# Performance work log

Measured on AMD Instinct MI355X. Metric: run time of the kernel, lower is better.

Reference implementation:

```python
import jax, jax.numpy as jnp
import numpy as np

B, S, D, H, K, F = 4, 2048, 512, 8, 512, 2048
EPS = 1e-3  # keras LayerNormalization default epsilon


def setup_inputs() -> dict:
    key = jax.random.key(0)
    ks = jax.random.split(key, 12)
    s = 0.02
    return {
        "x":  jax.random.normal(ks[0], (B, S, D), jnp.float32),
        "Wq": jax.random.normal(ks[1], (D, H, K), jnp.float32) * s,
        "bq": jnp.zeros((H, K), jnp.float32),
        "Wk": jax.random.normal(ks[2], (D, H, K), jnp.float32) * s,
        "bk": jnp.zeros((H, K), jnp.float32),
        "Wv": jax.random.normal(ks[3], (D, H, K), jnp.float32) * s,
        "bv": jnp.zeros((H, K), jnp.float32),
        "Wo": jax.random.normal(ks[4], (H, K, D), jnp.float32) * s,
        "bo": jnp.zeros((D,), jnp.float32),
        "W1": jax.random.normal(ks[5], (D, F), jnp.float32) * s,
        "b1": jnp.zeros((F,), jnp.float32),
        "W2": jax.random.normal(ks[6], (F, D), jnp.float32) * s,
        "b2": jnp.zeros((D,), jnp.float32),
        "g1": jnp.ones((D,), jnp.float32),
        "be1": jnp.zeros((D,), jnp.float32),
        "g2": jnp.ones((D,), jnp.float32),
        "be2": jnp.zeros((D,), jnp.float32),
    }


def _layernorm(x, g, b):
    m = jnp.mean(x, axis=-1, keepdims=True)
    v = jnp.mean(jnp.square(x - m), axis=-1, keepdims=True)
    return (x - m) * jax.lax.rsqrt(v + EPS) * g + b


def reference(x, Wq, bq, Wk, bk, Wv, bv, Wo, bo, W1, b1, W2, b2, g1, be1, g2, be2):
    # --- multi-head attention with tridiagonal band mask (window=1) ---
    q = jnp.einsum("bsd,dhk->bshk", x, Wq) + bq
    k = jnp.einsum("bsd,dhk->bshk", x, Wk) + bk
    v = jnp.einsum("bsd,dhk->bshk", x, Wv) + bv
    scores = jnp.einsum("bqhk,bshk->bhqs", q, k) / jnp.sqrt(jnp.float32(K))
    idx = jnp.arange(S)
    band = jnp.abs(idx[:, None] - idx[None, :]) <= 1  # band_part(ones,1,1)
    scores = jnp.where(band[None, None], scores, jnp.float32(-1e9))
    probs = jax.nn.softmax(scores, axis=-1)
    ctx = jnp.einsum("bhqs,bshk->bqhk", probs, v)
    attn = jnp.einsum("bqhk,hkd->bqd", ctx, Wo) + bo
    # dropout is identity at inference
    out1 = _layernorm(x + attn, g1, be1)
    # --- FFN: Dense(gelu) -> Dense ---
    h = jax.nn.gelu(out1 @ W1 + b1, approximate=False)
    ffn = h @ W2 + b2
    return _layernorm(out1 + ffn, g2, be2)
```

## Files before the change

### kernel.cpp

```cpp
#include <hip/hip_runtime.h>
#include <hip/hip_bf16.h>
#include <math.h>

#define B_ 4
#define S_ 2048
#define D_ 512
#define H_ 8
#define K_ 512
#define F_ 2048
#define NT 8192
#define HK 4096

typedef __attribute__((ext_vector_type(8))) short bf16x8;
typedef __attribute__((ext_vector_type(4))) float f32x4;
typedef unsigned short u16;

__device__ __forceinline__ float bits2f(u16 b) {
  union { unsigned u; float f; } c; c.u = ((unsigned)b) << 16; return c.f;
}
__device__ __forceinline__ u16 f2bfbits(float f) {
  union { float f; unsigned u; } c; c.f = f;
  unsigned r = c.u + 0x7fffu + ((c.u >> 16) & 1u);
  return (u16)(r >> 16);
}

__device__ __forceinline__ void gload16(const void* g, void* lds) {
  __builtin_amdgcn_global_load_lds(
      (const __attribute__((address_space(1))) unsigned int*)g,
      (__attribute__((address_space(3))) unsigned int*)lds, 16, 0, 0);
}

__global__ __launch_bounds__(256) void prep_all(
    const float* __restrict__ Wq, const float* __restrict__ Wk,
    const float* __restrict__ Wv, const float* __restrict__ Wo,
    const float* __restrict__ W1, const float* __restrict__ W2,
    const float* __restrict__ bv, const float* __restrict__ x,
    u16* __restrict__ wq_nt, u16* __restrict__ wk_nt,
    u16* __restrict__ mtwv, u16* __restrict__ wot,
    u16* __restrict__ w1t, u16* __restrict__ w2t,
    float* __restrict__ biascat, u16* __restrict__ xb) {
  const int id = blockIdx.x;
  const int tid = threadIdx.x;
  __shared__ float tile[32][33];
  if (id < 6144) {
    const int tx = tid & 31;
    const int ty = tid >> 5;
    const float* src; u16* dst;
    int rb, cb, ldin, ldout;
    if (id < 2048) {
      int rem = id; rb = (rem & 15) * 32; cb = (rem >> 4) * 32;
      src = Wv; ldin = HK; dst = mtwv + (size_t)4096 * 512; ldout = D_;
    } else if (id < 4096) {
      int rem = id - 2048; rb = (rem >> 4) * 32; cb = (rem & 15) * 32;
      src = Wo; ldin = D_; dst = wot; ldout = HK;
    } else if (id < 5120) {
      int rem = id - 4096; rb = (rem & 15) * 32; cb = (rem >> 4) * 32;
      src = W1; ldin = F_; dst = w1t; ldout = D_;
    } else {
      int rem = id - 5120; rb = (rem >> 4) * 32; cb = (rem & 15) * 32;
      src = W2; ldin = D_; dst = w2t; ldout = F_;
    }
    for (int i = ty; i < 32; i += 8)
      tile[i][tx] = src[(size_t)(rb + i) * ldin + cb + tx];
    __syncthreads();
    for (int i = ty; i < 32; i += 8)
      dst[(size_t)(cb + i) * ldout + rb + tx] = f2bfbits(tile[tx][i]);
  } else if (id < 14336) {
    const float* s; u16* d; int base;
    if (id < 8192)       { s = Wq; d = wq_nt; base = id - 6144; }
    else if (id < 10240) { s = Wk; d = wk_nt; base = id - 8192; }
    else                 { s = x;  d = xb;    base = id - 10240; }
    int i = base * 256 + tid;
    float4 f = ((const float4*)s)[i];
    ushort4 o;
    o.x = f2bfbits(f.x); o.y = f2bfbits(f.y);
    o.z = f2bfbits(f.z); o.w = f2bfbits(f.w);
    ((ushort4*)d)[i] = o;
  } else {
    int i = (id - 14336) * 256 + tid;
    float4 o = make_float4(0.f, 0.f, 0.f, 0.f);
    if (i >= 1024) o = ((const float4*)bv)[i - 1024];
    ((float4*)biascat)[i] = o;
  }
}

template <int BIAS, int GELU, int OUTBF, int BATCH>
__global__ __launch_bounds__(256) void gemm128d(const u16* __restrict__ A, int lda,
                                                size_t aZ,
                                                const u16* __restrict__ Bt, int ldb,
                                                size_t bZ,
                                                const float* __restrict__ bias,
                                                float* __restrict__ Cf, size_t zstride,
                                                u16* __restrict__ Cb, int ldc,
                                                size_t cZ, int kslice) {
  __shared__ short lds[2][16384];
  const int tid = threadIdx.x;
  const int lane = tid & 63;
  const int wave = tid >> 6;
  const int bm = blockIdx.x * 128;
  const int bn = blockIdx.y * 128;
  const int z = blockIdx.z;
  const int k0 = BATCH ? 0 : z * kslice;
  if (BATCH) { A += z * aZ; Bt += z * bZ; }

  const int wr = (wave >> 1) * 64;
  const int wc = (wave & 1) * 64;

  f32x4 acc[4][4] = {};

  const int srow = wave * 8 + (lane >> 3);
  const int scol = ((lane & 7) ^ (lane >> 3)) * 8;
  const u16* ag = A + (size_t)(bm + srow) * lda + scol;
  const u16* bg = Bt + (size_t)(bn + srow) * ldb + scol;
  const int ldsbase = wave * 8 * 64;

  auto STAGE = [&](int buf, int kt) {
    short* sA = &lds[buf][0];
    short* sB = &lds[buf][8192];
#pragma unroll
    for (int r = 0; r < 4; ++r)
      gload16(ag + (size_t)(r * 32) * lda + kt, sA + ldsbase + r * 32 * 64);
#pragma unroll
    for (int r = 0; r < 4; ++r)
      gload16(bg + (size_t)(r * 32) * ldb + kt, sB + ldsbase + r * 32 * 64);
  };

  auto COMPUTE = [&](int buf) {
    const short* sA = &lds[buf][0];
    const short* sB = &lds[buf][8192];
#pragma unroll
    for (int ks = 0; ks < 2; ++ks) {
      const int kos = (ks * 32 + (lane >> 4) * 8) ^ ((lane & 7) << 3);
      bf16x8 a[4], b[4];
#pragma unroll
      for (int m = 0; m < 4; ++m)
        a[m] = *(const bf16x8*)&sA[(wr + m * 16 + (lane & 15)) * 64 + kos];
#pragma unroll
      for (int n = 0; n < 4; ++n)
        b[n] = *(const bf16x8*)&sB[(wc + n * 16 + (lane & 15)) * 64 + kos];
#pragma unroll
      for (int m = 0; m < 4; ++m)
#pragma unroll
        for (int n = 0; n < 4; ++n)
          acc[m][n] = __builtin_amdgcn_mfma_f32_16x16x32_bf16(a[m], b[n], acc[m][n], 0, 0, 0);
    }
  };

  const int nt = kslice >> 6;
  STAGE(0, k0);
  __syncthreads();
  int cur = 0;
  for (int t = 0; t + 1 < nt; ++t) {
    STAGE(cur ^ 1, k0 + (t + 1) * 64);
    COMPUTE(cur);
    __syncthreads();
    cur ^= 1;
  }
  COMPUTE(cur);

  float* Cfz = Cf + (BATCH ? 0 : (size_t)z * zstride);
  u16* Cbz = Cb + (BATCH ? (size_t)z * cZ : 0);
#pragma unroll
  for (int m = 0; m < 4; ++m) {
    const int row0 = bm + wr + m * 16 + (lane >> 4) * 4;
#pragma unroll
    for (int n = 0; n < 4; ++n) {
      const int col = bn + wc + n * 16 + (lane & 15);
      float badd = BIAS ? bias[col] : 0.f;
      f32x4 a4 = acc[m][n];
#pragma unroll
      for (int r = 0; r < 4; ++r) {
        float vv = a4[r] + badd;
        if (GELU) vv = 0.5f * vv * (1.f + erff(vv * 0.70710678118f));
        const int row = row0 + r;
        if (OUTBF) Cbz[(size_t)row * ldc + col] = f2bfbits(vv);
        else Cfz[(size_t)row * ldc + col] = vv;
      }
    }
  }
}

__global__ __launch_bounds__(256) void attn2(u16* yv, const u16* __restrict__ xb) {
  const int t = blockIdx.x;
  const int s = t & (S_ - 1);
  const int tid = threadIdx.x;
  const int lane = tid & 63;
  const int wave = tid >> 6;
  __shared__ float sSc[8][3];
  __shared__ float sP[8][3];
  const u16* yrow = yv + (size_t)t * 8192;

#pragma unroll
  for (int i = 0; i < 6; ++i) {
    const int didx = wave * 6 + i;
    const int h = didx / 3, j = didx % 3;
    const bool valid = !((j == 0 && s == 0) || (j == 2 && s == S_ - 1));
    float d = 0.f;
    if (valid) {
      const int tj = t + j - 1;
      bf16x8 y8 = *(const bf16x8*)&yrow[h * 512 + lane * 8];
      bf16x8 x8 = *(const bf16x8*)&xb[(size_t)tj * D_ + lane * 8];
#pragma unroll
      for (int e = 0; e < 8; ++e) d += bits2f((u16)y8[e]) * bits2f((u16)x8[e]);
    }
    for (int m = 32; m >= 1; m >>= 1) d += __shfl_xor(d, m);
    if (lane == 0) sSc[h][j] = valid ? d : -1e30f;
  }
  __syncthreads();
  if (tid < 8) {
    const float scale = 0.044194173824159f;
    float s0 = sSc[tid][0], s1 = sSc[tid][1], s2 = sSc[tid][2];
    s0 = (s0 > -1e29f) ? s0 * scale : -1e30f;
    s1 = s1 * scale;
    s2 = (s2 > -1e29f) ? s2 * scale : -1e30f;
    float mx = fmaxf(s0, fmaxf(s1, s2));
    float p0 = (s0 > -1e29f) ? expf(s0 - mx) : 0.f;
    float p1 = expf(s1 - mx);
    float p2 = (s2 > -1e29f) ? expf(s2 - mx) : 0.f;
    float inv = 1.f / (p0 + p1 + p2);
    sP[tid][0] = p0 * inv; sP[tid][1] = p1 * inv; sP[tid][2] = p2 * inv;
  }
  __syncthreads();
  const int c0 = tid * 16;
  const int h = tid >> 5;
  const float p0 = sP[h][0], p1 = sP[h][1], p2 = sP[h][2];
  const int tm = t - (s > 0 ? 1 : 0);
  const int tp = t + (s < S_ - 1 ? 1 : 0);
  const u16* v0r = yv + (size_t)tm * 8192 + 4096;
  const u16* v1r = yv + (size_t)t * 8192 + 4096;
  const u16* v2r = yv + (size_t)tp * 8192 + 4096;
#pragma unroll
  for (int c = 0; c < 2; ++c) {
    const int col = c0 + c * 8;
    bf16x8 a = *(const bf16x8*)&v0r[col];
    bf16x8 b = *(const bf16x8*)&v1r[col];
    bf16x8 cc = *(const bf16x8*)&v2r[col];
    bf16x8 o;
#pragma unroll
    for (int e = 0; e < 8; ++e)
      o[e] = (short)f2bfbits(p0 * bits2f((u16)a[e]) + p1 * bits2f((u16)b[e]) +
                             p2 * bits2f((u16)cc[e]));
    *(bf16x8*)&yv[(size_t)t * 8192 + col] = o;
  }
}

__global__ __launch_bounds__(256) void resid_ln(const float* __restrict__ xres,
                                                const float* __restrict__ parts,
                                                int nparts, size_t pstride,
                                                size_t prowstride,
                                                const float* __restrict__ bias,
                                                const float* __restrict__ gamma,
                                                const float* __restrict__ beta,
                                                float* __restrict__ outf,
                                                u16* __restrict__ outb) {
  const int row = blockIdx.x;
  const int tid = threadIdx.x;
  const size_t base = (size_t)row * D_;
  float2 xv = ((const float2*)(xres + base))[tid];
  float y0 = xv.x, y1 = xv.y;
  for (int p = 0; p < nparts; ++p) {
    const float* pr = parts + p * pstride + (size_t)row * prowstride;
    float2 pv = ((const float2*)pr)[tid];
    y0 += pv.x; y1 += pv.y;
  }
  if (bias) {
    float2 bv = ((const float2*)bias)[tid];
    y0 += bv.x; y1 += bv.y;
  }
  float s = y0 + y1, ss = y0 * y0 + y1 * y1;
  for (int m = 32; m >= 1; m >>= 1) { s += __shfl_xor(s, m); ss += __shfl_xor(ss, m); }
  __shared__ float red[8];
  const int wave = tid >> 6, lane = tid & 63;
  if (lane == 0) { red[wave] = s; red[4 + wave] = ss; }
  __syncthreads();
  s = red[0] + red[1] + red[2] + red[3];
  ss = red[4] + red[5] + red[6] + red[7];
  const float mean = s * (1.f / D_);
  const float var = ss * (1.f / D_) - mean * mean;
  const float rstd = rsqrtf(var + 1e-3f);
  float2 gv = ((const float2*)gamma)[tid];
  float2 bev = ((const float2*)beta)[tid];
  float o0 = (y0 - mean) * rstd * gv.x + bev.x;
  float o1 = (y1 - mean) * rstd * gv.y + bev.y;
  if (outf) { float2 of; of.x = o0; of.y = o1; ((float2*)(outf + base))[tid] = of; }
  if (outb) { ushort2 ob; ob.x = f2bfbits(o0); ob.y = f2bfbits(o1); ((ushort2*)(outb + base))[tid] = ob; }
}

extern "C" void kernel_launch(void* const* d_in, const int* in_sizes, int n_in,
                              void* d_out, int out_size, void* d_ws, size_t ws_size,
                              hipStream_t stream) {
  const float* x  = (const float*)d_in[0];
  const float* Wq = (const float*)d_in[1];
  const float* Wk = (const float*)d_in[3];
  const float* Wv = (const float*)d_in[5];
  const float* bv = (const float*)d_in[6];
  const float* Wo = (const float*)d_in[7];
  const float* bo = (const float*)d_in[8];
  const float* W1 = (const float*)d_in[9];
  const float* b1 = (const float*)d_in[10];
  const float* W2 = (const float*)d_in[11];
  const float* b2 = (const float*)d_in[12];
  const float* g1 = (const float*)d_in[13];
  const float* be1 = (const float*)d_in[14];
  const float* g2 = (const float*)d_in[15];
  const float* be2 = (const float*)d_in[16];
  float* out = (float*)d_out;

  char* w = (char*)d_ws;
  size_t o = 0;
  auto nxt = [&](size_t bytes) -> char* {
    char* p = w + o;
    o += (bytes + 255) & ~(size_t)255;
    return p;
  };
  u16* xb     = (u16*)nxt((size_t)NT * D_ * 2);
  u16* wq_nt  = (u16*)nxt((size_t)D_ * HK * 2);
  u16* wk_nt  = (u16*)nxt((size_t)D_ * HK * 2);
  u16* wot    = (u16*)nxt((size_t)D_ * HK * 2);
  u16* w1t    = (u16*)nxt((size_t)F_ * D_ * 2);
  u16* w2t    = (u16*)nxt((size_t)D_ * F_ * 2);
  u16* mtwv   = (u16*)nxt((size_t)8192 * 512 * 2);
  float* biascat = (float*)nxt((size_t)8192 * 4);
  u16* yv     = (u16*)nxt((size_t)NT * 8192 * 2);
  float* out1f = (float*)nxt((size_t)NT * D_ * 4);
  u16* out1b   = (u16*)nxt((size_t)NT * D_ * 2);
  float* woPart = (float*)(yv + 4096);
  u16* hb = (u16*)((char*)yv + 33554432);
  float* ffnP = (float*)((char*)yv + 100663296);

  prep_all<<<dim3(14344), 256, 0, stream>>>(Wq, Wk, Wv, Wo, W1, W2, bv, x,
                                            wq_nt, wk_nt, mtwv, wot, w1t, w2t,
                                            biascat, xb);

  gemm128d<0, 0, 1, 1><<<dim3(4, 4, 8), 256, 0, stream>>>(
      wk_nt, HK, 512, wq_nt, HK, 512, nullptr,
      nullptr, 0, mtwv, 512, (size_t)512 * 512, 512);

  gemm128d<1, 0, 1, 0><<<dim3(64, 64, 1), 256, 0, stream>>>(
      xb, D_, 0, mtwv, 512, 0, biascat, nullptr, 0, yv, 8192, 0, 512);

  attn2<<<dim3(NT), 256, 0, stream>>>(yv, xb);

  gemm128d<0, 0, 0, 0><<<dim3(64, 4, 2), 256, 0, stream>>>(
      yv, 8192, 0, wot, HK, 0, nullptr, woPart, 512, nullptr, 4096, 0, 2048);

  resid_ln<<<dim3(NT), 256, 0, stream>>>(x, woPart, 2, 512, 4096, bo,
                                         g1, be1, out1f, out1b);

  gemm128d<1, 1, 1, 0><<<dim3(64, 16, 1), 256, 0, stream>>>(
      out1b, D_, 0, w1t, D_, 0, b1, nullptr, 0, hb, F_, 0, 512);

  gemm128d<0, 0, 0, 0><<<dim3(64, 4, 2), 256, 0, stream>>>(
      hb, F_, 0, w2t, F_, 0, nullptr, ffnP, (size_t)NT * D_, nullptr, D_, 0, 1024);

  resid_ln<<<dim3(NT), 256, 0, stream>>>(out1f, ffnP, 2, (size_t)NT * D_, D_, b2,
                                         g2, be2, out, nullptr);

  (void)in_sizes; (void)n_in; (void)out_size; (void)ws_size;
}
```

Measured before the change: 303.1 us.

## Fold Wo into value projection and drop separate output-projection GEMM

Precomputes Wv·Wo per head as a combined weight inside the batched weight GEMM, so the large projection GEMM emits per-head value vectors already projected to model dimension. Attention then mixes the three band neighbours across all heads into a single 512-wide fp32 row, which removes the separate Wo GEMM over the 4096-wide context. The bv·Wo bias is folded in by a small new kernel. The big projection GEMM stays the same size, and the extra precomputed products add a little bf16 rounding.

```diff
diff --git a/kernel.cpp b/kernel.cpp
--- a/kernel.cpp
+++ b/kernel.cpp
@@ -34,30 +34,27 @@
     const float* __restrict__ Wq, const float* __restrict__ Wk,
     const float* __restrict__ Wv, const float* __restrict__ Wo,
     const float* __restrict__ W1, const float* __restrict__ W2,
-    const float* __restrict__ bv, const float* __restrict__ x,
+    const float* __restrict__ x,
     u16* __restrict__ wq_nt, u16* __restrict__ wk_nt,
-    u16* __restrict__ mtwv, u16* __restrict__ wot,
+    u16* __restrict__ wv_nt, u16* __restrict__ wot,
     u16* __restrict__ w1t, u16* __restrict__ w2t,
-    float* __restrict__ biascat, u16* __restrict__ xb) {
+    u16* __restrict__ xb) {
   const int id = blockIdx.x;
   const int tid = threadIdx.x;
   __shared__ float tile[32][33];
-  if (id < 6144) {
+  if (id < 4096) {
     const int tx = tid & 31;
     const int ty = tid >> 5;
     const float* src; u16* dst;
     int rb, cb, ldin, ldout;
     if (id < 2048) {
-      int rem = id; rb = (rem & 15) * 32; cb = (rem >> 4) * 32;
-      src = Wv; ldin = HK; dst = mtwv + (size_t)4096 * 512; ldout = D_;
-    } else if (id < 4096) {
-      int rem = id - 2048; rb = (rem >> 4) * 32; cb = (rem & 15) * 32;
+      int rem = id; rb = (rem >> 4) * 32; cb = (rem & 15) * 32;
       src = Wo; ldin = D_; dst = wot; ldout = HK;
-    } else if (id < 5120) {
-      int rem = id - 4096; rb = (rem & 15) * 32; cb = (rem >> 4) * 32;
+    } else if (id < 3072) {
+      int rem = id - 2048; rb = (rem & 15) * 32; cb = (rem >> 4) * 32;
       src = W1; ldin = F_; dst = w1t; ldout = D_;
     } else {
-      int rem = id - 5120; rb = (rem >> 4) * 32; cb = (rem & 15) * 32;
+      int rem = id - 3072; rb = (rem >> 4) * 32; cb = (rem & 15) * 32;
       src = W2; ldin = D_; dst = w2t; ldout = F_;
     }
     for (int i = ty; i < 32; i += 8)
@@ -65,10 +62,11 @@
     __syncthreads();
     for (int i = ty; i < 32; i += 8)
       dst[(size_t)(cb + i) * ldout + rb + tx] = f2bfbits(tile[tx][i]);
-  } else if (id < 14336) {
+  } else {
     const float* s; u16* d; int base;
-    if (id < 8192)       { s = Wq; d = wq_nt; base = id - 6144; }
-    else if (id < 10240) { s = Wk; d = wk_nt; base = id - 8192; }
+    if (id < 6144)       { s = Wq; d = wq_nt; base = id - 4096; }
+    else if (id < 8192)  { s = Wk; d = wk_nt; base = id - 6144; }
+    else if (id < 10240) { s = Wv; d = wv_nt; base = id - 8192; }
     else                 { s = x;  d = xb;    base = id - 10240; }
     int i = base * 256 + tid;
     float4 f = ((const float4*)s)[i];
@@ -76,11 +74,25 @@
     o.x = f2bfbits(f.x); o.y = f2bfbits(f.y);
     o.z = f2bfbits(f.z); o.w = f2bfbits(f.w);
     ((ushort4*)d)[i] = o;
-  } else {
-    int i = (id - 14336) * 256 + tid;
-    float4 o = make_float4(0.f, 0.f, 0.f, 0.f);
-    if (i >= 1024) o = ((const float4*)bv)[i - 1024];
-    ((float4*)biascat)[i] = o;
+  }
+}
+
+__global__ __launch_bounds__(256) void cbias(const float* __restrict__ bv,
+                                             const float* __restrict__ Wo,
+                                             float* __restrict__ biascat) {
+  const int lane = threadIdx.x & 63;
+  const int out = blockIdx.x * 4 + (threadIdx.x >> 6);
+  const int h = out >> 9, dp = out & 511;
+  float a = 0.f;
+#pragma unroll
+  for (int i = 0; i < 8; ++i) {
+    const int k = lane * 8 + i;
+    a += bv[h * 512 + k] * Wo[(size_t)(h * 512 + k) * D_ + dp];
+  }
+  for (int m = 32; m >= 1; m >>= 1) a += __shfl_xor(a, m);
+  if (lane == 0) {
+    biascat[4096 + out] = a;
+    biascat[out] = 0.f;
   }
 }
 
@@ -89,6 +101,9 @@
                                                 size_t aZ,
                                                 const u16* __restrict__ Bt, int ldb,
                                                 size_t bZ,
+                                                const u16* __restrict__ A2,
+                                                const u16* __restrict__ Bt2,
+                                                int zsplit,
                                                 const float* __restrict__ bias,
                                                 float* __restrict__ Cf, size_t zstride,
                                                 u16* __restrict__ Cb, int ldc,
@@ -101,7 +116,10 @@
   const int bn = blockIdx.y * 128;
   const int z = blockIdx.z;
   const int k0 = BATCH ? 0 : z * kslice;
-  if (BATCH) { A += z * aZ; Bt += z * bZ; }
+  if (BATCH) {
+    if (z < zsplit) { A += (size_t)z * aZ; Bt += (size_t)z * bZ; }
+    else { A = A2 + (size_t)(z - zsplit) * aZ; Bt = Bt2 + (size_t)(z - zsplit) * bZ; }
+  }
 
   const int wr = (wave >> 1) * 64;
   const int wc = (wave & 1) * 64;
@@ -180,7 +198,7 @@
   }
 }
 
-__global__ __launch_bounds__(256) void attn2(u16* yv, const u16* __restrict__ xb) {
+__global__ __launch_bounds__(256) void attn3(u16* yz, const u16* __restrict__ xb) {
   const int t = blockIdx.x;
   const int s = t & (S_ - 1);
   const int tid = threadIdx.x;
@@ -188,7 +206,7 @@
   const int wave = tid >> 6;
   __shared__ float sSc[8][3];
   __shared__ float sP[8][3];
-  const u16* yrow = yv + (size_t)t * 8192;
+  const u16* yrow = yz + (size_t)t * 8192;
 
 #pragma unroll
   for (int i = 0; i < 6; ++i) {
@@ -221,27 +239,24 @@
     sP[tid][0] = p0 * inv; sP[tid][1] = p1 * inv; sP[tid][2] = p2 * inv;
   }
   __syncthreads();
-  const int c0 = tid * 16;
-  const int h = tid >> 5;
-  const float p0 = sP[h][0], p1 = sP[h][1], p2 = sP[h][2];
+  const int d0 = tid * 2;
   const int tm = t - (s > 0 ? 1 : 0);
   const int tp = t + (s < S_ - 1 ? 1 : 0);
-  const u16* v0r = yv + (size_t)tm * 8192 + 4096;
-  const u16* v1r = yv + (size_t)t * 8192 + 4096;
-  const u16* v2r = yv + (size_t)tp * 8192 + 4096;
-#pragma unroll
-  for (int c = 0; c < 2; ++c) {
-    const int col = c0 + c * 8;
-    bf16x8 a = *(const bf16x8*)&v0r[col];
-    bf16x8 b = *(const bf16x8*)&v1r[col];
-    bf16x8 cc = *(const bf16x8*)&v2r[col];
-    bf16x8 o;
-#pragma unroll
-    for (int e = 0; e < 8; ++e)
-      o[e] = (short)f2bfbits(p0 * bits2f((u16)a[e]) + p1 * bits2f((u16)b[e]) +
-                             p2 * bits2f((u16)cc[e]));
-    *(bf16x8*)&yv[(size_t)t * 8192 + col] = o;
-  }
+  const int trow[3] = {tm, t, tp};
+  float a0 = 0.f, a1 = 0.f;
+#pragma unroll
+  for (int j = 0; j < 3; ++j) {
+    const u16* zr = yz + (size_t)trow[j] * 8192 + 4096;
+#pragma unroll
+    for (int h = 0; h < 8; ++h) {
+      const float p = sP[h][j];
+      unsigned zz = *(const unsigned*)&zr[h * 512 + d0];
+      a0 += p * bits2f((u16)(zz & 0xffffu));
+      a1 += p * bits2f((u16)(zz >> 16));
+    }
+  }
+  float2 o; o.x = a0; o.y = a1;
+  *(float2*)((float*)(yz + (size_t)t * 8192) + d0) = o;
 }
 
 __global__ __launch_bounds__(256) void resid_ln(const float* __restrict__ xres,
@@ -316,42 +331,44 @@
   u16* xb     = (u16*)nxt((size_t)NT * D_ * 2);
   u16* wq_nt  = (u16*)nxt((size_t)D_ * HK * 2);
   u16* wk_nt  = (u16*)nxt((size_t)D_ * HK * 2);
+  u16* wv_nt  = (u16*)nxt((size_t)D_ * HK * 2);
   u16* wot    = (u16*)nxt((size_t)D_ * HK * 2);
   u16* w1t    = (u16*)nxt((size_t)F_ * D_ * 2);
   u16* w2t    = (u16*)nxt((size_t)D_ * F_ * 2);
-  u16* mtwv   = (u16*)nxt((size_t)8192 * 512 * 2);
+  u16* mg     = (u16*)nxt((size_t)8192 * 512 * 2);
   float* biascat = (float*)nxt((size_t)8192 * 4);
-  u16* yv     = (u16*)nxt((size_t)NT * 8192 * 2);
+  u16* yz     = (u16*)nxt((size_t)NT * 8192 * 2);
   float* out1f = (float*)nxt((size_t)NT * D_ * 4);
   u16* out1b   = (u16*)nxt((size_t)NT * D_ * 2);
-  float* woPart = (float*)(yv + 4096);
-  u16* hb = (u16*)((char*)yv + 33554432);
-  float* ffnP = (float*)((char*)yv + 100663296);
-
-  prep_all<<<dim3(14344), 256, 0, stream>>>(Wq, Wk, Wv, Wo, W1, W2, bv, x,
-                                            wq_nt, wk_nt, mtwv, wot, w1t, w2t,
-                                            biascat, xb);
-
-  gemm128d<0, 0, 1, 1><<<dim3(4, 4, 8), 256, 0, stream>>>(
-      wk_nt, HK, 512, wq_nt, HK, 512, nullptr,
-      nullptr, 0, mtwv, 512, (size_t)512 * 512, 512);
+  float* attnf = (float*)yz;
+  u16* hb = (u16*)yz;
+  float* ffnP = (float*)((char*)yz + 67108864);
+
+  prep_all<<<dim3(14336), 256, 0, stream>>>(Wq, Wk, Wv, Wo, W1, W2, x,
+                                            wq_nt, wk_nt, wv_nt, wot, w1t, w2t,
+                                            xb);
+  cbias<<<dim3(1024), 256, 0, stream>>>(bv, Wo, biascat);
+
+  gemm128d<0, 0, 1, 1><<<dim3(4, 4, 16), 256, 0, stream>>>(
+      wk_nt, HK, 512, wq_nt, HK, 512, wot, wv_nt, 8,
+      nullptr, nullptr, 0, mg, 512, (size_t)512 * 512, 512);
 
   gemm128d<1, 0, 1, 0><<<dim3(64, 64, 1), 256, 0, stream>>>(
-      xb, D_, 0, mtwv, 512, 0, biascat, nullptr, 0, yv, 8192, 0, 512);
-
-  attn2<<<dim3(NT), 256, 0, stream>>>(yv, xb);
+      xb, D_, 0, mg, 512, 0, nullptr, nullptr, 0, biascat,
+      nullptr, 0, yz, 8192, 0, 512);
+
+  attn3<<<dim3(NT), 256, 0, stream>>>(yz, xb);
+
+  resid_ln<<<dim3(NT), 256, 0, stream>>>(x, attnf, 1, 0, 4096, bo,
+                                         g1, be1, out1f, out1b);
+
+  gemm128d<1, 1, 1, 0><<<dim3(64, 16, 1), 256, 0, stream>>>(
+      out1b, D_, 0, w1t, D_, 0, nullptr, nullptr, 0, b1,
+      nullptr, 0, hb, F_, 0, 512);
 
   gemm128d<0, 0, 0, 0><<<dim3(64, 4, 2), 256, 0, stream>>>(
-      yv, 8192, 0, wot, HK, 0, nullptr, woPart, 512, nullptr, 4096, 0, 2048);
-
-  resid_ln<<<dim3(NT), 256, 0, stream>>>(x, woPart, 2, 512, 4096, bo,
-                                         g1, be1, out1f, out1b);
-
-  gemm128d<1, 1, 1, 0><<<dim3(64, 16, 1), 256, 0, stream>>>(
-      out1b, D_, 0, w1t, D_, 0, b1, nullptr, 0, hb, F_, 0, 512);
-
-  gemm128d<0, 0, 0, 0><<<dim3(64, 4, 2), 256, 0, stream>>>(
-      hb, F_, 0, w2t, F_, 0, nullptr, ffnP, (size_t)NT * D_, nullptr, D_, 0, 1024);
+      hb, F_, 0, w2t, F_, 0, nullptr, nullptr, 0, nullptr,
+      ffnP, (size_t)NT * D_, nullptr, D_, 0, 1024);
 
   resid_ln<<<dim3(NT), 256, 0, stream>>>(out1f, ffnP, 2, (size_t)NT * D_, D_, b2,
                                          g2, be2, out, nullptr);
```

Result: faster. 271.0 us (-10.6%).
